# Kernel optimization log

Hardware: AMD Instinct MI355X
Metric: run time of the kernel (lower is better)

Reference implementation:

```python
import jax, jax.numpy as jnp
import numpy as np

B, C, S, HID = 64, 512, 28, 256  # batch, channels, spatial size, LSTM hidden


def _param(k, shape):
    return jax.random.normal(k, shape, jnp.float32) * 0.05


def setup_inputs() -> dict:
    key = jax.random.key(0)
    ks = jax.random.split(key, 19)
    inp = {"x": jax.random.normal(ks[0], (B, C, S, S), jnp.float32)}
    # vertical bidirectional LSTM (input C, hidden HID), torch gate order i,f,g,o
    inp["v_wih_f"] = _param(ks[1], (4 * HID, C))
    inp["v_whh_f"] = _param(ks[2], (4 * HID, HID))
    inp["v_b_f"] = _param(ks[3], (4 * HID,))
    inp["v_wih_b"] = _param(ks[4], (4 * HID, C))
    inp["v_whh_b"] = _param(ks[5], (4 * HID, HID))
    inp["v_b_b"] = _param(ks[6], (4 * HID,))
    # horizontal bidirectional LSTM (input 2*HID=512, hidden HID)
    inp["h_wih_f"] = _param(ks[7], (4 * HID, 2 * HID))
    inp["h_whh_f"] = _param(ks[8], (4 * HID, HID))
    inp["h_b_f"] = _param(ks[9], (4 * HID,))
    inp["h_wih_b"] = _param(ks[10], (4 * HID, 2 * HID))
    inp["h_whh_b"] = _param(ks[11], (4 * HID, HID))
    inp["h_b_b"] = _param(ks[12], (4 * HID,))
    # 1x1 conv 512 -> 100 (10x10 attention kernel logits)
    inp["conv_w"] = _param(ks[13], (100, 2 * HID))
    inp["conv_b"] = _param(ks[14], (100,))
    return inp


def _lstm_scan(xs, wih, whh, b):
    # xs: [T, N, D] -> h sequence [T, N, HID]
    hdim = whh.shape[1]
    def step(carry, xt):
        h, c = carry
        gates = xt @ wih.T + h @ whh.T + b  # [N, 4H]
        i, f, g, o = jnp.split(gates, 4, axis=-1)
        c = jax.nn.sigmoid(f) * c + jax.nn.sigmoid(i) * jnp.tanh(g)
        h = jax.nn.sigmoid(o) * jnp.tanh(c)
        return (h, c), h
    n = xs.shape[1]
    z = jnp.zeros((n, hdim), xs.dtype)
    _, hs = jax.lax.scan(step, (z, z), xs)
    return hs


def _bilstm(x, wf, uf, bf, wb, ub, bb):
    # x: [N, T, D] -> [N, T, 2*HID]
    xs = jnp.swapaxes(x, 0, 1)
    hf = _lstm_scan(xs, wf, uf, bf)
    hb = _lstm_scan(xs[::-1], wb, ub, bb)[::-1]
    return jnp.swapaxes(jnp.concatenate([hf, hb], axis=-1), 0, 1)


def reference(x, v_wih_f, v_whh_f, v_b_f, v_wih_b, v_whh_b, v_b_b,
              h_wih_f, h_whh_f, h_b_f, h_wih_b, h_whh_b, h_b_b,
              conv_w, conv_b):
    b, c, s, _ = x.shape
    xt = jnp.transpose(x, (0, 3, 2, 1))            # [B, W, H, C]
    # vertical LSTM: seq over W, batched over (B, H)
    v_in = jnp.transpose(xt, (0, 2, 1, 3)).reshape(b * s, s, c)
    v_out = _bilstm(v_in, v_wih_f, v_whh_f, v_b_f, v_wih_b, v_whh_b, v_b_b)
    v_out = jnp.transpose(v_out.reshape(b, s, s, 2 * HID), (0, 2, 1, 3))  # [B, W, H, 512]
    # horizontal LSTM: seq over H, batched over (B, W)
    h_in = v_out.reshape(b * s, s, 2 * HID)
    h_out = _bilstm(h_in, h_wih_f, h_whh_f, h_b_f, h_wih_b, h_whh_b, h_b_b)
    feat = jnp.transpose(h_out.reshape(b, s, s, 2 * HID), (0, 3, 2, 1))  # [B, 512, H, W]
    # 1x1 conv -> [B, 100, H, W], softmax over 100 kernel entries
    kern = jnp.einsum('bfhw,of->bohw', feat, conv_w) + conv_b[None, :, None, None]
    kern = jax.nn.softmax(kern, axis=1)
    # faithful to torch: C-order reshape [B,100,H,W] -> (B*H*W, 100) kernels
    w = kern.reshape(b, s * s, 100)
    # grouped dilated conv3d == weighted sum over dilation-3 sampled 10x10 grid
    x_s = x[:, :, ::3, ::3].reshape(b, c, 100)     # [B, C, 100]
    out = jnp.einsum('bpk,bck->bpc', w, x_s)       # [B, H*W, C]
    return out.reshape(b, c, s, s)                 # faithful C-order reshape
```

## Files before the change

kernel.cpp:

```cpp
#include <hip/hip_runtime.h>
#include <hip/hip_bf16.h>
#include <stdint.h>

typedef __hip_bfloat16 bf16_t;
typedef __attribute__((ext_vector_type(8))) short short8;
typedef __attribute__((ext_vector_type(4))) float f32x4;
typedef __attribute__((ext_vector_type(4))) unsigned int u32x4;

#define MFMA16(a, b, c) __builtin_amdgcn_mfma_f32_16x16x32_bf16(a, b, c, 0, 0, 0)

#define NROW 50176
#define NBATCH 1792

__device__ __forceinline__ void g2l16(const void* g, void* l) {
  __builtin_amdgcn_global_load_lds(
      (const __attribute__((address_space(1))) unsigned int*)g,
      (__attribute__((address_space(3))) unsigned int*)l, 16, 0, 0);
}
__device__ __forceinline__ float sigm(float x) { return 1.0f / (1.0f + __expf(-x)); }
__device__ __forceinline__ float tanh_(float x) { return 2.0f / (1.0f + __expf(-2.0f * x)) - 1.0f; }
__device__ __forceinline__ void stc(bf16_t* p, float v) { *p = __float2bfloat16(v); }
__device__ __forceinline__ void stc(float* p, float v) { *p = v; }
__device__ __forceinline__ float bf2f(unsigned short u) {
  return __uint_as_float((unsigned int)u << 16);
}

struct CvtArgs {
  const float* src[8];
  bf16_t* dst[8];
  int n[8];
};
__global__ void cvt_all(CvtArgs a) {
  int arr = blockIdx.y;
  int i = blockIdx.x * 256 + threadIdx.x;
  if (i < a.n[arr]) a.dst[arr][i] = __float2bfloat16(a.src[arr][i]);
}

__global__ void transpose_x(const float* __restrict__ x, bf16_t* __restrict__ Xin) {
  int c0 = blockIdx.x * 128, h = blockIdx.y, b = blockIdx.z;
  __shared__ __align__(16) short tile[128 * 29];
  const float* xb = x + ((size_t)b * 512 + c0) * 784 + h * 28;
  for (int e = threadIdx.x; e < 128 * 28; e += 256) {
    int cc = e / 28, w = e - cc * 28;
    tile[cc * 29 + w] = __bfloat16_as_short(__float2bfloat16(xb[(size_t)cc * 784 + w]));
  }
  __syncthreads();
  size_t orow0 = (size_t)(b * 28 + h) * 28;
  short* os = (short*)Xin;
  for (int e = threadIdx.x; e < 28 * 128; e += 256) {
    int w = e >> 7, cc = e & 127;
    int c = c0 + cc;
    os[(size_t)(c >> 5) * NROW * 32 + (orow0 + w) * 32 + (c & 31)] = tile[cc * 29 + w];
  }
}

__global__ void build_xs(const float* __restrict__ x, bf16_t* __restrict__ xs) {
  int c = blockIdx.x, b = blockIdx.y;
  int k = threadIdx.x;
  const float* xr = x + ((size_t)b * 512 + c) * 784;
  float v = 0.0f;
  if (k < 100) { int kh = k / 10, kw = k - kh * 10; v = xr[kh * 84 + kw * 3]; }
  xs[((size_t)b * 512 + c) * 128 + k] = __float2bfloat16(v);
}

__global__ void pad_conv(const float* __restrict__ cw, const float* __restrict__ cb,
                         bf16_t* __restrict__ cwp, float* __restrict__ cbp,
                         unsigned int* __restrict__ bar) {
  int r = blockIdx.x;
  if (r == 0)
    for (int i = threadIdx.x; i < 1792; i += 128) bar[i] = 0;
  for (int i = threadIdx.x; i < 512; i += 128)
    cwp[r * 512 + i] = __float2bfloat16((r < 100) ? cw[r * 512 + i] : 0.0f);
  if (r == 0) cbp[threadIdx.x] = (threadIdx.x < 100) ? cb[threadIdx.x] : 0.0f;
}

template <typename CT, bool CPERM>
__global__ __launch_bounds__(256) void gemm_bt(
    const bf16_t* __restrict__ A, const bf16_t* __restrict__ B0,
    const bf16_t* __restrict__ B1, const float* __restrict__ bias0,
    const float* __restrict__ bias1, CT* __restrict__ C, int M, int N, int K) {
  __shared__ __align__(16) short As[128 * 32];
  __shared__ __align__(16) short Bs[128 * 32];
  int tid = threadIdx.x;
  int nb = blockIdx.x;
  int bm0 = blockIdx.y * 128, bn0 = nb * 128;
  int lrow = tid >> 2, lseg = tid & 3;
  const char* Ag = (const char*)A + ((size_t)(bm0 + lrow) * 32 + lseg * 8) * 2;
  size_t Aadv = (size_t)M * 64;
  const float* biasp;
  const char *Bg1, *Bg2;
  int js = 0;
  if (CPERM) {
    int dir = nb >> 3;
    js = nb & 7;
    const bf16_t* Bsel = dir ? B1 : B0;
    biasp = dir ? bias1 : bias0;
    int br1 = (lrow >> 5) * 256 + js * 32 + (lrow & 31);
    int br2 = ((lrow + 64) >> 5) * 256 + js * 32 + (lrow & 31);
    Bg1 = (const char*)(B0 + 0, Bsel + (size_t)br1 * K) + lseg * 16;
    Bg2 = (const char*)(Bsel + (size_t)br2 * K) + lseg * 16;
  } else {
    biasp = bias0 + bn0;
    Bg1 = (const char*)(B0 + (size_t)(bn0 + lrow) * K) + lseg * 16;
    Bg2 = Bg1 + (size_t)64 * K * 2;
  }
  int w = tid >> 6, l = tid & 63, lm = l & 15, lq = l >> 4;
  int wm = w & 1, wn = w >> 1;
  f32x4 acc[4][4] = {};
  for (int k0 = 0; k0 < K; k0 += 32) {
    g2l16(Ag, (char*)As + tid * 16);
    g2l16(Ag + 4096, (char*)As + 4096 + tid * 16);
    g2l16(Bg1, (char*)Bs + tid * 16);
    g2l16(Bg2, (char*)Bs + 4096 + tid * 16);
    Ag += Aadv; Bg1 += 64; Bg2 += 64;
    __syncthreads();
    short8 afr[4], bfr[4];
#pragma unroll
    for (int i = 0; i < 4; i++) {
      afr[i] = *(const short8*)&As[(wm * 64 + i * 16 + lm) * 32 + lq * 8];
      bfr[i] = *(const short8*)&Bs[(wn * 64 + i * 16 + lm) * 32 + lq * 8];
    }
#pragma unroll
    for (int mi = 0; mi < 4; mi++)
#pragma unroll
      for (int ni = 0; ni < 4; ni++) acc[mi][ni] = MFMA16(afr[mi], bfr[ni], acc[mi][ni]);
    __syncthreads();
  }
  float bv[4];
#pragma unroll
  for (int ni = 0; ni < 4; ni++) {
    int cb = wn * 64 + ni * 16 + lm;
    bv[ni] = CPERM ? biasp[(cb >> 5) * 256 + js * 32 + (cb & 31)] : biasp[cb];
  }
#pragma unroll
  for (int mi = 0; mi < 4; mi++)
#pragma unroll
    for (int ni = 0; ni < 4; ni++) {
      int col = bn0 + wn * 64 + ni * 16 + lm;
#pragma unroll
      for (int r = 0; r < 4; r++) {
        size_t row = bm0 + wm * 64 + mi * 16 + lq * 4 + r;
        stc(&C[row * N + col], acc[mi][ni][r] + bv[ni]);
      }
    }
}

__global__ __launch_bounds__(256, 2) void lstm_scan(
    const bf16_t* __restrict__ G, const bf16_t* __restrict__ whh_f,
    const bf16_t* __restrict__ whh_b, bf16_t* __restrict__ hA,
    bf16_t* __restrict__ hB, bf16_t* __restrict__ outb,
    unsigned int* __restrict__ bar) {
  int dir = blockIdx.y;
  int js = blockIdx.x & 7;
  int rg = blockIdx.x >> 3;
  int tid = threadIdx.x, w = tid >> 6, l = tid & 63, lm = l & 15, lq = l >> 4;
  const short* whh = (const short*)(dir ? whh_b : whh_f);
  __shared__ __align__(16) short Ws[128 * 256];
  __shared__ __align__(16) short ht[64 * 40];
#pragma unroll
  for (int i = 0; i < 16; i++) {
    int segid = i * 256 + tid;
    int row = segid >> 5, seg = segid & 31;
    int gate = row >> 5, jj = row & 31;
    short8 v = *(const short8*)&whh[((size_t)(gate * 256 + js * 32 + jj)) * 256 + seg * 8];
    *(short8*)&Ws[row * 256 + ((seg ^ (row & 7)) * 8)] = v;
  }
  __syncthreads();
  unsigned int* cnt = bar + (dir * 28 + rg) * 16;
  int r0 = rg * 64 + w * 16;
  size_t dbase = (size_t)dir * 458752;
  const unsigned short* Gb = (const unsigned short*)G + (size_t)dir * 1024 + js * 128;
  float creg[2][4] = {};
  unsigned short gvs[2][4][4];
  auto load_gvs = [&](int tt) {
#pragma unroll
    for (int nj = 0; nj < 2; nj++)
#pragma unroll
      for (int r = 0; r < 4; r++) {
        int bi = r0 + lq * 4 + r;
        const unsigned short* gp = Gb + ((size_t)bi * 28 + tt) * 2048 + nj * 16 + lm;
#pragma unroll
        for (int gate = 0; gate < 4; gate++) gvs[nj][gate][r] = gp[gate * 32];
      }
  };
  load_gvs(dir ? 27 : 0);
#pragma unroll 1
  for (int s = 0; s < 28; s++) {
    int t = dir ? 27 - s : s;
    f32x4 acc[4][2] = {};
    if (s > 0) {
      const unsigned long long* hrp =
          (const unsigned long long*)((s & 1) ? hA : hB);
      unsigned long long hq[8][2];
#pragma unroll
      for (int kk = 0; kk < 8; kk++) {
        size_t off = dbase + (size_t)kk * 57344 + (size_t)(r0 + lm) * 32 + lq * 8;
        hq[kk][0] =
            __hip_atomic_load(hrp + (off >> 2), __ATOMIC_RELAXED, __HIP_MEMORY_SCOPE_AGENT);
        hq[kk][1] = __hip_atomic_load(hrp + (off >> 2) + 1, __ATOMIC_RELAXED,
                                      __HIP_MEMORY_SCOPE_AGENT);
      }
#pragma unroll
      for (int kk = 0; kk < 8; kk++) {
        short8 a;
        ((unsigned long long*)&a)[0] = hq[kk][0];
        ((unsigned long long*)&a)[1] = hq[kk][1];
        int bseg = ((kk * 4 + lq) ^ (lm & 7)) * 8;
#pragma unroll
        for (int gate = 0; gate < 4; gate++)
#pragma unroll
          for (int nj = 0; nj < 2; nj++) {
            short8 b = *(const short8*)&Ws[(gate * 32 + nj * 16 + lm) * 256 + bseg];
            acc[gate][nj] = MFMA16(a, b, acc[gate][nj]);
          }
      }
    }
#pragma unroll
    for (int nj = 0; nj < 2; nj++)
#pragma unroll
      for (int r = 0; r < 4; r++) {
        float gi = bf2f(gvs[nj][0][r]) + acc[0][nj][r];
        float gf = bf2f(gvs[nj][1][r]) + acc[1][nj][r];
        float gg = bf2f(gvs[nj][2][r]) + acc[2][nj][r];
        float go = bf2f(gvs[nj][3][r]) + acc[3][nj][r];
        float cn = sigm(gf) * creg[nj][r] + sigm(gi) * tanh_(gg);
        float hn = sigm(go) * tanh_(cn);
        creg[nj][r] = cn;
        ht[(w * 16 + lq * 4 + r) * 40 + nj * 16 + lm] =
            __bfloat16_as_short(__float2bfloat16(hn));
      }
    if (s < 27) load_gvs(dir ? 26 - s : s + 1);
    __syncthreads();
    {
      int row = tid >> 2, seg = tid & 3;
      u32x4 v = *(const u32x4*)&ht[row * 40 + seg * 8];
      int bi = rg * 64 + row;
      unsigned long long* hwp = (unsigned long long*)((s & 1) ? hB : hA);
      size_t off = dbase + (size_t)js * 57344 + (size_t)bi * 32 + seg * 8;
      unsigned long long q0 = ((const unsigned long long*)&v)[0];
      unsigned long long q1 = ((const unsigned long long*)&v)[1];
      __hip_atomic_store(hwp + (off >> 2), q0, __ATOMIC_RELAXED, __HIP_MEMORY_SCOPE_AGENT);
      __hip_atomic_store(hwp + (off >> 2) + 1, q1, __ATOMIC_RELAXED,
                         __HIP_MEMORY_SCOPE_AGENT);
      int bb = bi / 28, rr = bi - bb * 28;
      short* ob = (short*)outb + (size_t)(dir * 8 + js) * NROW * 32;
      *(u32x4*)&ob[((size_t)bb * 784 + (size_t)t * 28 + rr) * 32 + seg * 8] = v;
    }
    if (s < 27) {
      asm volatile("s_waitcnt vmcnt(0)" ::: "memory");
      __syncthreads();
      if (tid == 0) {
        __hip_atomic_fetch_add(cnt, 1u, __ATOMIC_RELAXED, __HIP_MEMORY_SCOPE_AGENT);
        unsigned int tgt = 8u * (unsigned)(s + 1);
        while (__hip_atomic_load(cnt, __ATOMIC_RELAXED, __HIP_MEMORY_SCOPE_AGENT) < tgt)
          __builtin_amdgcn_s_sleep(2);
      }
      __syncthreads();
      __builtin_amdgcn_sched_barrier(0);
    }
  }
}

__global__ void softmax_scatter(const float* __restrict__ P, bf16_t* __restrict__ Wscr) {
  int row = blockIdx.x;
  int l = threadIdx.x;
  int b = row / 784, q = row - b * 784;
  const float* pr = P + (size_t)row * 128;
  float v0 = (l < 100) ? pr[l] : -1e30f;
  float v1 = (l + 64 < 100) ? pr[l + 64] : -1e30f;
  float m = fmaxf(v0, v1);
  for (int off = 32; off > 0; off >>= 1) m = fmaxf(m, __shfl_down(m, off));
  m = __shfl(m, 0);
  float e0 = (l < 100) ? __expf(v0 - m) : 0.0f;
  float e1 = (l + 64 < 100) ? __expf(v1 - m) : 0.0f;
  float sum = e0 + e1;
  for (int off = 32; off > 0; off >>= 1) sum += __shfl_down(sum, off);
  sum = __shfl(sum, 0);
  float inv = 1.0f / sum;
  size_t base = (size_t)b * 784 * 128;
  if (l < 100) {
    int mm = l * 784 + q;
    Wscr[base + (size_t)(mm / 100) * 128 + (mm % 100)] = __float2bfloat16(e0 * inv);
  }
  int o = l + 64;
  if (o < 100) {
    int mm = o * 784 + q;
    Wscr[base + (size_t)(mm / 100) * 128 + (mm % 100)] = __float2bfloat16(e1 * inv);
  }
}

__global__ __launch_bounds__(256) void final_gemm(const bf16_t* __restrict__ Wscr,
                                                  const bf16_t* __restrict__ xs,
                                                  float* __restrict__ outp) {
  int m0 = blockIdx.x * 112, n0 = blockIdx.y * 128, b = blockIdx.z;
  int tid = threadIdx.x, w = tid >> 6, l = tid & 63, lm = l & 15, lq = l >> 4;
  const short* Ab = (const short*)Wscr + (size_t)b * 784 * 128;
  const short* Bb = (const short*)xs + (size_t)b * 512 * 128;
  f32x4 acc[7][2] = {};
#pragma unroll
  for (int kk = 0; kk < 4; kk++) {
    short8 b0 = *(const short8*)&Bb[(size_t)(n0 + w * 32 + lm) * 128 + kk * 32 + lq * 8];
    short8 b1 = *(const short8*)&Bb[(size_t)(n0 + w * 32 + 16 + lm) * 128 + kk * 32 + lq * 8];
#pragma unroll
    for (int mi = 0; mi < 7; mi++) {
      short8 a = *(const short8*)&Ab[(size_t)(m0 + mi * 16 + lm) * 128 + kk * 32 + lq * 8];
      acc[mi][0] = MFMA16(a, b0, acc[mi][0]);
      acc[mi][1] = MFMA16(a, b1, acc[mi][1]);
    }
  }
#pragma unroll
  for (int mi = 0; mi < 7; mi++)
#pragma unroll
    for (int ni = 0; ni < 2; ni++) {
      int c = n0 + w * 32 + ni * 16 + lm;
#pragma unroll
      for (int r = 0; r < 4; r++) {
        int p = m0 + mi * 16 + lq * 4 + r;
        outp[(size_t)b * 401408 + (size_t)p * 512 + c] = acc[mi][ni][r];
      }
    }
}

extern "C" void kernel_launch(void* const* d_in, const int* in_sizes, int n_in,
                              void* d_out, int out_size, void* d_ws, size_t ws_size,
                              hipStream_t stream) {
  const float* x = (const float*)d_in[0];
  const float* v_wih_f = (const float*)d_in[1];
  const float* v_whh_f = (const float*)d_in[2];
  const float* v_b_f = (const float*)d_in[3];
  const float* v_wih_b = (const float*)d_in[4];
  const float* v_whh_b = (const float*)d_in[5];
  const float* v_b_b = (const float*)d_in[6];
  const float* h_wih_f = (const float*)d_in[7];
  const float* h_whh_f = (const float*)d_in[8];
  const float* h_b_f = (const float*)d_in[9];
  const float* h_wih_b = (const float*)d_in[10];
  const float* h_whh_b = (const float*)d_in[11];
  const float* h_b_b = (const float*)d_in[12];
  const float* conv_w = (const float*)d_in[13];
  const float* conv_b = (const float*)d_in[14];

  char* ws = (char*)d_ws;
  bf16_t* Xin = (bf16_t*)(ws);
  bf16_t* Vout = (bf16_t*)(ws + 51380224);
  bf16_t* G = (bf16_t*)(ws + 102760448);
  float* P = (float*)(ws + 102760448);
  bf16_t* Wscr = (bf16_t*)(ws + 128450560);
  bf16_t* xs = (bf16_t*)(ws + 308281344);
  bf16_t* cwp = (bf16_t*)(ws + 316669952);
  float* cbp = (float*)(ws + 316801024);
  bf16_t* hstate = (bf16_t*)(ws + 316801536);
  unsigned int* bar = (unsigned int*)(ws + 318636544);
  bf16_t* wvf = (bf16_t*)(ws + 322306560);
  bf16_t* wvb = (bf16_t*)(ws + 323355136);
  bf16_t* uvf = (bf16_t*)(ws + 324403712);
  bf16_t* uvb = (bf16_t*)(ws + 324928000);
  bf16_t* whf = (bf16_t*)(ws + 325452288);
  bf16_t* whb = (bf16_t*)(ws + 326500864);
  bf16_t* uhf = (bf16_t*)(ws + 327549440);
  bf16_t* uhb = (bf16_t*)(ws + 328073728);
  bf16_t* Hout = Xin;

  CvtArgs ca;
  ca.src[0] = v_wih_f; ca.dst[0] = wvf; ca.n[0] = 524288;
  ca.src[1] = v_wih_b; ca.dst[1] = wvb; ca.n[1] = 524288;
  ca.src[2] = v_whh_f; ca.dst[2] = uvf; ca.n[2] = 262144;
  ca.src[3] = v_whh_b; ca.dst[3] = uvb; ca.n[3] = 262144;
  ca.src[4] = h_wih_f; ca.dst[4] = whf; ca.n[4] = 524288;
  ca.src[5] = h_wih_b; ca.dst[5] = whb; ca.n[5] = 524288;
  ca.src[6] = h_whh_f; ca.dst[6] = uhf; ca.n[6] = 262144;
  ca.src[7] = h_whh_b; ca.dst[7] = uhb; ca.n[7] = 262144;
  cvt_all<<<dim3(2048, 8), 256, 0, stream>>>(ca);

  transpose_x<<<dim3(4, 28, 64), 256, 0, stream>>>(x, Xin);
  build_xs<<<dim3(512, 64), 128, 0, stream>>>(x, xs);
  pad_conv<<<dim3(128), 128, 0, stream>>>(conv_w, conv_b, cwp, cbp, bar);

  gemm_bt<bf16_t, true><<<dim3(16, 392), 256, 0, stream>>>(
      Xin, wvf, wvb, v_b_f, v_b_b, G, NROW, 2048, 512);
  lstm_scan<<<dim3(224, 2), 256, 0, stream>>>(G, uvf, uvb, hstate, Xin, Vout, bar);

  gemm_bt<bf16_t, true><<<dim3(16, 392), 256, 0, stream>>>(
      Vout, whf, whb, h_b_f, h_b_b, G, NROW, 2048, 512);
  lstm_scan<<<dim3(224, 2), 256, 0, stream>>>(G, uhf, uhb, hstate, Vout, Hout, bar + 896);

  gemm_bt<float, false><<<dim3(1, 392), 256, 0, stream>>>(
      Hout, cwp, cwp, cbp, cbp, P, NROW, 128, 512);
  softmax_scatter<<<dim3(50176), 64, 0, stream>>>(P, Wscr);
  final_gemm<<<dim3(7, 4, 64), 256, 0, stream>>>(Wscr, xs, (float*)d_out);
}
```

Baseline: 1.044 ms.

## Interleave gate columns in input GEMM output and prefetch gate preactivations earlier

```diff
diff --git a/kernel.cpp b/kernel.cpp
--- a/kernel.cpp
+++ b/kernel.cpp
@@ -4,8 +4,10 @@
 
 typedef __hip_bfloat16 bf16_t;
 typedef __attribute__((ext_vector_type(8))) short short8;
+typedef __attribute__((ext_vector_type(4))) short short4v;
 typedef __attribute__((ext_vector_type(4))) float f32x4;
 typedef __attribute__((ext_vector_type(4))) unsigned int u32x4;
+typedef unsigned long long ull;
 
 #define MFMA16(a, b, c) __builtin_amdgcn_mfma_f32_16x16x32_bf16(a, b, c, 0, 0, 0)
 
@@ -95,9 +97,9 @@
     js = nb & 7;
     const bf16_t* Bsel = dir ? B1 : B0;
     biasp = dir ? bias1 : bias0;
-    int br1 = (lrow >> 5) * 256 + js * 32 + (lrow & 31);
-    int br2 = ((lrow + 64) >> 5) * 256 + js * 32 + (lrow & 31);
-    Bg1 = (const char*)(B0 + 0, Bsel + (size_t)br1 * K) + lseg * 16;
+    int br1 = (lrow & 3) * 256 + js * 32 + (lrow >> 2);
+    int br2 = br1 + 16;
+    Bg1 = (const char*)(Bsel + (size_t)br1 * K) + lseg * 16;
     Bg2 = (const char*)(Bsel + (size_t)br2 * K) + lseg * 16;
   } else {
     biasp = bias0 + bn0;
@@ -130,7 +132,7 @@
 #pragma unroll
   for (int ni = 0; ni < 4; ni++) {
     int cb = wn * 64 + ni * 16 + lm;
-    bv[ni] = CPERM ? biasp[(cb >> 5) * 256 + js * 32 + (cb & 31)] : biasp[cb];
+    bv[ni] = CPERM ? biasp[(cb & 3) * 256 + js * 32 + (cb >> 2)] : biasp[cb];
   }
 #pragma unroll
   for (int mi = 0; mi < 4; mi++)
@@ -169,42 +171,59 @@
   unsigned int* cnt = bar + (dir * 28 + rg) * 16;
   int r0 = rg * 64 + w * 16;
   size_t dbase = (size_t)dir * 458752;
-  const unsigned short* Gb = (const unsigned short*)G + (size_t)dir * 1024 + js * 128;
+
+  const unsigned short* gb[2][4];
+#pragma unroll
+  for (int nj = 0; nj < 2; nj++)
+#pragma unroll
+    for (int r = 0; r < 4; r++) {
+      int bi = r0 + lq * 4 + r;
+      gb[nj][r] = (const unsigned short*)G + (size_t)bi * 28 * 2048 + (size_t)dir * 1024 +
+                  js * 128 + (nj * 16 + lm) * 4;
+    }
+  size_t hro = (dbase + (size_t)(r0 + lm) * 32 + lq * 8) >> 2;
+  int srow = tid >> 2, sseg = tid & 3;
+  int sbi = rg * 64 + srow;
+  size_t hwo = (dbase + (size_t)js * 57344 + (size_t)sbi * 32 + sseg * 8) >> 2;
+  int sbb = sbi / 28, srr = sbi - sbb * 28;
+  short* obase = (short*)outb + (size_t)(dir * 8 + js) * NROW * 32 +
+                 ((size_t)sbb * 784 + srr) * 32 + sseg * 8;
+
   float creg[2][4] = {};
-  unsigned short gvs[2][4][4];
-  auto load_gvs = [&](int tt) {
+  ull gq[2][4], gqn[2][4];
+  {
+    size_t tofs = (size_t)(dir ? 27 : 0) * 2048;
 #pragma unroll
     for (int nj = 0; nj < 2; nj++)
 #pragma unroll
-      for (int r = 0; r < 4; r++) {
-        int bi = r0 + lq * 4 + r;
-        const unsigned short* gp = Gb + ((size_t)bi * 28 + tt) * 2048 + nj * 16 + lm;
-#pragma unroll
-        for (int gate = 0; gate < 4; gate++) gvs[nj][gate][r] = gp[gate * 32];
-      }
-  };
-  load_gvs(dir ? 27 : 0);
+      for (int r = 0; r < 4; r++) gq[nj][r] = *(const ull*)(gb[nj][r] + tofs);
+  }
 #pragma unroll 1
   for (int s = 0; s < 28; s++) {
     int t = dir ? 27 - s : s;
     f32x4 acc[4][2] = {};
     if (s > 0) {
-      const unsigned long long* hrp =
-          (const unsigned long long*)((s & 1) ? hA : hB);
-      unsigned long long hq[8][2];
+      const ull* hrp = (const ull*)((s & 1) ? hA : hB);
+      ull hq[8][2];
 #pragma unroll
       for (int kk = 0; kk < 8; kk++) {
-        size_t off = dbase + (size_t)kk * 57344 + (size_t)(r0 + lm) * 32 + lq * 8;
-        hq[kk][0] =
-            __hip_atomic_load(hrp + (off >> 2), __ATOMIC_RELAXED, __HIP_MEMORY_SCOPE_AGENT);
-        hq[kk][1] = __hip_atomic_load(hrp + (off >> 2) + 1, __ATOMIC_RELAXED,
-                                      __HIP_MEMORY_SCOPE_AGENT);
+        size_t o = hro + (size_t)kk * 14336;
+        hq[kk][0] = __hip_atomic_load(hrp + o, __ATOMIC_RELAXED, __HIP_MEMORY_SCOPE_AGENT);
+        hq[kk][1] =
+            __hip_atomic_load(hrp + o + 1, __ATOMIC_RELAXED, __HIP_MEMORY_SCOPE_AGENT);
+      }
+      if (s < 27) {
+        size_t tofs = (size_t)(dir ? 26 - s : s + 1) * 2048;
+#pragma unroll
+        for (int nj = 0; nj < 2; nj++)
+#pragma unroll
+          for (int r = 0; r < 4; r++) gqn[nj][r] = *(const ull*)(gb[nj][r] + tofs);
       }
 #pragma unroll
       for (int kk = 0; kk < 8; kk++) {
         short8 a;
-        ((unsigned long long*)&a)[0] = hq[kk][0];
-        ((unsigned long long*)&a)[1] = hq[kk][1];
+        ((ull*)&a)[0] = hq[kk][0];
+        ((ull*)&a)[1] = hq[kk][1];
         int bseg = ((kk * 4 + lq) ^ (lm & 7)) * 8;
 #pragma unroll
         for (int gate = 0; gate < 4; gate++)
@@ -214,37 +233,37 @@
             acc[gate][nj] = MFMA16(a, b, acc[gate][nj]);
           }
       }
+    } else {
+      size_t tofs = (size_t)(dir ? 26 : 1) * 2048;
+#pragma unroll
+      for (int nj = 0; nj < 2; nj++)
+#pragma unroll
+        for (int r = 0; r < 4; r++) gqn[nj][r] = *(const ull*)(gb[nj][r] + tofs);
     }
 #pragma unroll
     for (int nj = 0; nj < 2; nj++)
 #pragma unroll
       for (int r = 0; r < 4; r++) {
-        float gi = bf2f(gvs[nj][0][r]) + acc[0][nj][r];
-        float gf = bf2f(gvs[nj][1][r]) + acc[1][nj][r];
-        float gg = bf2f(gvs[nj][2][r]) + acc[2][nj][r];
-        float go = bf2f(gvs[nj][3][r]) + acc[3][nj][r];
+        short4v g4 = *(short4v*)&gq[nj][r];
+        float gi = bf2f((unsigned short)g4[0]) + acc[0][nj][r];
+        float gf = bf2f((unsigned short)g4[1]) + acc[1][nj][r];
+        float gg = bf2f((unsigned short)g4[2]) + acc[2][nj][r];
+        float go = bf2f((unsigned short)g4[3]) + acc[3][nj][r];
         float cn = sigm(gf) * creg[nj][r] + sigm(gi) * tanh_(gg);
         float hn = sigm(go) * tanh_(cn);
         creg[nj][r] = cn;
         ht[(w * 16 + lq * 4 + r) * 40 + nj * 16 + lm] =
             __bfloat16_as_short(__float2bfloat16(hn));
       }
-    if (s < 27) load_gvs(dir ? 26 - s : s + 1);
     __syncthreads();
     {
-      int row = tid >> 2, seg = tid & 3;
-      u32x4 v = *(const u32x4*)&ht[row * 40 + seg * 8];
-      int bi = rg * 64 + row;
-      unsigned long long* hwp = (unsigned long long*)((s & 1) ? hB : hA);
-      size_t off = dbase + (size_t)js * 57344 + (size_t)bi * 32 + seg * 8;
-      unsigned long long q0 = ((const unsigned long long*)&v)[0];
-      unsigned long long q1 = ((const unsigned long long*)&v)[1];
-      __hip_atomic_store(hwp + (off >> 2), q0, __ATOMIC_RELAXED, __HIP_MEMORY_SCOPE_AGENT);
-      __hip_atomic_store(hwp + (off >> 2) + 1, q1, __ATOMIC_RELAXED,
-                         __HIP_MEMORY_SCOPE_AGENT);
-      int bb = bi / 28, rr = bi - bb * 28;
-      short* ob = (short*)outb + (size_t)(dir * 8 + js) * NROW * 32;
-      *(u32x4*)&ob[((size_t)bb * 784 + (size_t)t * 28 + rr) * 32 + seg * 8] = v;
+      u32x4 v = *(const u32x4*)&ht[srow * 40 + sseg * 8];
+      ull* hwp = (ull*)((s & 1) ? hB : hA);
+      ull q0 = ((const ull*)&v)[0];
+      ull q1 = ((const ull*)&v)[1];
+      __hip_atomic_store(hwp + hwo, q0, __ATOMIC_RELAXED, __HIP_MEMORY_SCOPE_AGENT);
+      __hip_atomic_store(hwp + hwo + 1, q1, __ATOMIC_RELAXED, __HIP_MEMORY_SCOPE_AGENT);
+      *(u32x4*)(obase + (size_t)t * 896) = v;
     }
     if (s < 27) {
       asm volatile("s_waitcnt vmcnt(0)" ::: "memory");
@@ -257,6 +276,10 @@
       }
       __syncthreads();
       __builtin_amdgcn_sched_barrier(0);
+#pragma unroll
+      for (int nj = 0; nj < 2; nj++)
+#pragma unroll
+        for (int r = 0; r < 4; r++) gq[nj][r] = gqn[nj][r];
     }
   }
 }
```

New measurement: 1.054 ms. About the same (+1.0%).
